# Performance work log

Hardware: AMD Instinct MI355X
Metric: run time of the kernel (lower is better)

The kernel has to match this reference:

```python
import jax, jax.numpy as jnp
import numpy as np

TAU = 0.2
EPS_NORM = 1e-12  # torch F.normalize eps


def _l2_normalize(x):
    n = jnp.linalg.norm(x, axis=-1, keepdims=True)
    return x / jnp.maximum(n, EPS_NORM)


def setup_inputs() -> dict:
    key = jax.random.key(0)
    k1, k2 = jax.random.split(key)
    seg_emb = jax.random.normal(k1, (131072, 512), dtype=jnp.float32)
    prototypes = jax.random.normal(k2, (64, 512), dtype=jnp.float32) * 0.02
    return {"seg_emb": seg_emb, "prototypes": prototypes}


def reference(seg_emb, prototypes):
    # normalize -> cosine-sim matmul -> temperature scale -> softmax -> weighted proto sum
    p = _l2_normalize(prototypes)          # [K, D]
    z = _l2_normalize(seg_emb)             # [N, D]
    logits = jnp.einsum('nd,kd->nk', z, p) / max(TAU, 1e-06)  # [N, K]
    w = jax.nn.softmax(logits, axis=-1)    # [N, K]
    pattern = jnp.einsum('nk,kd->nd', w, prototypes)           # [N, D]
    return pattern, w, logits
```

## Files before the change

### kernel.cpp

```cpp
#include <hip/hip_runtime.h>
#include <hip/hip_bf16.h>

typedef __attribute__((ext_vector_type(8))) short short8;
typedef __attribute__((ext_vector_type(4))) float f32x4;

#define NPROTO 64
#define DIM    512
#define TAU_INV 5.0f

__device__ __forceinline__ unsigned short f2bf(float f) {
    union { float f; unsigned int u; } v; v.f = f;
    unsigned int r = v.u + 0x7FFFu + ((v.u >> 16) & 1u);
    return (unsigned short)(r >> 16);
}

__global__ void pb_prep(const float* __restrict__ protos,
                        unsigned short* __restrict__ pnorm,
                        unsigned short* __restrict__ protosT) {
    const int k    = blockIdx.x;
    const int lane = threadIdx.x;
    const float* row = protos + k * DIM;
    float x[8];
    float ss = 0.0f;
#pragma unroll
    for (int j = 0; j < 8; ++j) {
        x[j] = row[lane * 8 + j];
        ss += x[j] * x[j];
    }
#pragma unroll
    for (int m = 1; m < 64; m <<= 1) ss += __shfl_xor(ss, m, 64);
    const float s = 1.0f / fmaxf(sqrtf(ss), 1e-12f);
    short8 pn;
#pragma unroll
    for (int j = 0; j < 8; ++j) pn[j] = (short)f2bf(x[j] * s);
    *reinterpret_cast<short8*>(pnorm + k * DIM + lane * 8) = pn;
#pragma unroll
    for (int j = 0; j < 8; ++j)
        protosT[(lane * 8 + j) * NPROTO + k] = f2bf(x[j]);
}

__global__ __launch_bounds__(256, 4) void pb_main(
    const float* __restrict__ seg,
    const unsigned short* __restrict__ pnorm,
    const unsigned short* __restrict__ protosT,
    float* __restrict__ out_pat,
    float* __restrict__ out_w,
    float* __restrict__ out_log) {

    __shared__ unsigned short wbuf_all[4 * 2 * 16 * 64];

    const int wid  = (int)(threadIdx.x >> 6);
    const int lane = (int)(threadIdx.x & 63);
    const int g    = lane >> 4;
    const int r16  = lane & 15;
    const long n0  = ((long)blockIdx.x * 4 + wid) * 32;

    f32x4 acc0[4] = {}, acc1[4] = {};
    float ss0 = 0.0f, ss1 = 0.0f;
    const float* ap0 = seg + (n0 + r16) * DIM + g * 8;
    const float* ap1 = ap0 + 16 * DIM;

    f32x4 a00 = *reinterpret_cast<const f32x4*>(ap0);
    f32x4 a01 = *reinterpret_cast<const f32x4*>(ap0 + 4);
    f32x4 a10 = *reinterpret_cast<const f32x4*>(ap1);
    f32x4 a11 = *reinterpret_cast<const f32x4*>(ap1 + 4);

#pragma unroll
    for (int kt = 0; kt < 16; ++kt) {
        f32x4 n00, n01, n10, n11;
        if (kt < 15) {
            n00 = *reinterpret_cast<const f32x4*>(ap0 + (kt + 1) * 32);
            n01 = *reinterpret_cast<const f32x4*>(ap0 + (kt + 1) * 32 + 4);
            n10 = *reinterpret_cast<const f32x4*>(ap1 + (kt + 1) * 32);
            n11 = *reinterpret_cast<const f32x4*>(ap1 + (kt + 1) * 32 + 4);
        }
        short8 af0, af1;
#pragma unroll
        for (int j = 0; j < 4; ++j) {
            ss0 += a00[j] * a00[j] + a01[j] * a01[j];
            ss1 += a10[j] * a10[j] + a11[j] * a11[j];
            af0[j] = (short)f2bf(a00[j]); af0[j + 4] = (short)f2bf(a01[j]);
            af1[j] = (short)f2bf(a10[j]); af1[j + 4] = (short)f2bf(a11[j]);
        }
        const unsigned short* bbase = pnorm + r16 * DIM + g * 8 + kt * 32;
#pragma unroll
        for (int c = 0; c < 4; ++c) {
            const short8 bf = *reinterpret_cast<const short8*>(bbase + c * 16 * DIM);
            acc0[c] = __builtin_amdgcn_mfma_f32_16x16x32_bf16(af0, bf, acc0[c], 0, 0, 0);
            acc1[c] = __builtin_amdgcn_mfma_f32_16x16x32_bf16(af1, bf, acc1[c], 0, 0, 0);
        }
        if (kt < 15) { a00 = n00; a01 = n01; a10 = n10; a11 = n11; }
    }

    ss0 += __shfl_xor(ss0, 16, 64); ss0 += __shfl_xor(ss0, 32, 64);
    ss1 += __shfl_xor(ss1, 16, 64); ss1 += __shfl_xor(ss1, 32, 64);
    const float sco0 = TAU_INV / fmaxf(sqrtf(ss0), 1e-12f);
    const float sco1 = TAU_INV / fmaxf(sqrtf(ss1), 1e-12f);
    float sc0[4], sc1[4];
#pragma unroll
    for (int q = 0; q < 4; ++q) {
        sc0[q] = __shfl(sco0, g * 4 + q, 64);
        sc1[q] = __shfl(sco1, g * 4 + q, 64);
    }

    float lg0[4][4], lg1[4][4];
#pragma unroll
    for (int c = 0; c < 4; ++c)
#pragma unroll
        for (int q = 0; q < 4; ++q) {
            lg0[c][q] = acc0[c][q] * sc0[q];
            lg1[c][q] = acc1[c][q] * sc1[q];
            out_log[(n0 + g * 4 + q) * NPROTO + c * 16 + r16]      = lg0[c][q];
            out_log[(n0 + 16 + g * 4 + q) * NPROTO + c * 16 + r16] = lg1[c][q];
        }

    float w0[4][4], w1[4][4];
#pragma unroll
    for (int q = 0; q < 4; ++q) {
        float mx0 = fmaxf(fmaxf(lg0[0][q], lg0[1][q]), fmaxf(lg0[2][q], lg0[3][q]));
        float mx1 = fmaxf(fmaxf(lg1[0][q], lg1[1][q]), fmaxf(lg1[2][q], lg1[3][q]));
#pragma unroll
        for (int msk = 1; msk < 16; msk <<= 1) {
            mx0 = fmaxf(mx0, __shfl_xor(mx0, msk, 64));
            mx1 = fmaxf(mx1, __shfl_xor(mx1, msk, 64));
        }
        float e0[4], e1[4], sum0 = 0.0f, sum1 = 0.0f;
#pragma unroll
        for (int c = 0; c < 4; ++c) {
            e0[c] = __expf(lg0[c][q] - mx0); sum0 += e0[c];
            e1[c] = __expf(lg1[c][q] - mx1); sum1 += e1[c];
        }
#pragma unroll
        for (int msk = 1; msk < 16; msk <<= 1) {
            sum0 += __shfl_xor(sum0, msk, 64);
            sum1 += __shfl_xor(sum1, msk, 64);
        }
        const float i0 = 1.0f / sum0, i1 = 1.0f / sum1;
#pragma unroll
        for (int c = 0; c < 4; ++c) { w0[c][q] = e0[c] * i0; w1[c][q] = e1[c] * i1; }
    }

    unsigned short* wb0 = wbuf_all + (wid * 2 + 0) * (16 * 64);
    unsigned short* wb1 = wbuf_all + (wid * 2 + 1) * (16 * 64);
#pragma unroll
    for (int c = 0; c < 4; ++c)
#pragma unroll
        for (int q = 0; q < 4; ++q) {
            out_w[(n0 + g * 4 + q) * NPROTO + c * 16 + r16]      = w0[c][q];
            out_w[(n0 + 16 + g * 4 + q) * NPROTO + c * 16 + r16] = w1[c][q];
            const int row  = g * 4 + q;
            const int col  = c * 16 + r16;
            const int byte = (row * 128 + col * 2) ^ ((row & 7) << 4);
            *reinterpret_cast<unsigned short*>(reinterpret_cast<char*>(wb0) + byte) = f2bf(w0[c][q]);
            *reinterpret_cast<unsigned short*>(reinterpret_cast<char*>(wb1) + byte) = f2bf(w1[c][q]);
        }

    __syncthreads();

    short8 wa[2][2];
    {
        const int row = r16;
        const int b0 = (row * 128 + g * 16)      ^ ((row & 7) << 4);
        const int b1 = (row * 128 + g * 16 + 64) ^ ((row & 7) << 4);
        wa[0][0] = *reinterpret_cast<const short8*>(reinterpret_cast<char*>(wb0) + b0);
        wa[0][1] = *reinterpret_cast<const short8*>(reinterpret_cast<char*>(wb0) + b1);
        wa[1][0] = *reinterpret_cast<const short8*>(reinterpret_cast<char*>(wb1) + b0);
        wa[1][1] = *reinterpret_cast<const short8*>(reinterpret_cast<char*>(wb1) + b1);
    }

#pragma unroll 2
    for (int cp = 0; cp < 32; ++cp) {
        const unsigned short* bp = protosT + (cp * 16 + r16) * NPROTO + g * 8;
        const short8 b0 = *reinterpret_cast<const short8*>(bp);
        const short8 b1 = *reinterpret_cast<const short8*>(bp + 32);
        f32x4 p0 = {}, p1 = {};
        p0 = __builtin_amdgcn_mfma_f32_16x16x32_bf16(wa[0][0], b0, p0, 0, 0, 0);
        p0 = __builtin_amdgcn_mfma_f32_16x16x32_bf16(wa[0][1], b1, p0, 0, 0, 0);
        p1 = __builtin_amdgcn_mfma_f32_16x16x32_bf16(wa[1][0], b0, p1, 0, 0, 0);
        p1 = __builtin_amdgcn_mfma_f32_16x16x32_bf16(wa[1][1], b1, p1, 0, 0, 0);
#pragma unroll
        for (int q = 0; q < 4; ++q) {
            out_pat[(n0 + g * 4 + q) * DIM + cp * 16 + r16]      = p0[q];
            out_pat[(n0 + 16 + g * 4 + q) * DIM + cp * 16 + r16] = p1[q];
        }
    }
}

extern "C" void kernel_launch(void* const* d_in, const int* in_sizes, int n_in,
                              void* d_out, int out_size, void* d_ws, size_t ws_size,
                              hipStream_t stream) {
    const float* seg    = (const float*)d_in[0];
    const float* protos = (const float*)d_in[1];
    const int N = in_sizes[0] / DIM;

    float* out     = (float*)d_out;
    float* out_pat = out;
    float* out_w   = out_pat + (size_t)N * DIM;
    float* out_log = out_w + (size_t)N * NPROTO;

    unsigned short* pnorm   = (unsigned short*)d_ws;
    unsigned short* protosT = pnorm + NPROTO * DIM;

    pb_prep<<<NPROTO, 64, 0, stream>>>(protos, pnorm, protosT);
    pb_main<<<N / 128, 256, 0, stream>>>(seg, pnorm, protosT, out_pat, out_w, out_log);
}
```

Before: 167.6 us.

## Use nontemporal loads/stores, smaller blocks, XCD-aware block remap, prefetch proto tiles

The main kernel now uses nontemporal loads for the embedding stream and nontemporal stores for all three outputs, to avoid polluting caches with single-use data. Blocks shrink from 4 to 2 waves, and block indices are remapped so that consecutive row chunks land on the same XCD. The redundant __syncthreads is removed, since each wave only reads its own LDS region. The transposed-prototype fragments are double-buffered in registers during the second matmul. The kernel is memory-bound, so most of the effect depends on how the cache hints and the block remap interact with HBM traffic. The remap silently assumes the grid size is a multiple of 8.

```diff
diff --git a/kernel.cpp b/kernel.cpp
--- a/kernel.cpp
+++ b/kernel.cpp
@@ -39,7 +39,7 @@
         protosT[(lane * 8 + j) * NPROTO + k] = f2bf(x[j]);
 }
 
-__global__ __launch_bounds__(256, 4) void pb_main(
+__global__ __launch_bounds__(128, 4) void pb_main(
     const float* __restrict__ seg,
     const unsigned short* __restrict__ pnorm,
     const unsigned short* __restrict__ protosT,
@@ -47,32 +47,36 @@
     float* __restrict__ out_w,
     float* __restrict__ out_log) {
 
-    __shared__ unsigned short wbuf_all[4 * 2 * 16 * 64];
+    __shared__ unsigned short wbuf_all[2 * 2 * 16 * 64];
 
     const int wid  = (int)(threadIdx.x >> 6);
     const int lane = (int)(threadIdx.x & 63);
     const int g    = lane >> 4;
     const int r16  = lane & 15;
-    const long n0  = ((long)blockIdx.x * 4 + wid) * 32;
+
+    const int nwg  = (int)gridDim.x;
+    const int cpx  = nwg >> 3;
+    const int blk  = ((int)blockIdx.x & 7) * cpx + ((int)blockIdx.x >> 3);
+    const long n0  = ((long)blk * 2 + wid) * 32;
 
     f32x4 acc0[4] = {}, acc1[4] = {};
     float ss0 = 0.0f, ss1 = 0.0f;
     const float* ap0 = seg + (n0 + r16) * DIM + g * 8;
     const float* ap1 = ap0 + 16 * DIM;
 
-    f32x4 a00 = *reinterpret_cast<const f32x4*>(ap0);
-    f32x4 a01 = *reinterpret_cast<const f32x4*>(ap0 + 4);
-    f32x4 a10 = *reinterpret_cast<const f32x4*>(ap1);
-    f32x4 a11 = *reinterpret_cast<const f32x4*>(ap1 + 4);
+    f32x4 a00 = __builtin_nontemporal_load(reinterpret_cast<const f32x4*>(ap0));
+    f32x4 a01 = __builtin_nontemporal_load(reinterpret_cast<const f32x4*>(ap0 + 4));
+    f32x4 a10 = __builtin_nontemporal_load(reinterpret_cast<const f32x4*>(ap1));
+    f32x4 a11 = __builtin_nontemporal_load(reinterpret_cast<const f32x4*>(ap1 + 4));
 
 #pragma unroll
     for (int kt = 0; kt < 16; ++kt) {
         f32x4 n00, n01, n10, n11;
         if (kt < 15) {
-            n00 = *reinterpret_cast<const f32x4*>(ap0 + (kt + 1) * 32);
-            n01 = *reinterpret_cast<const f32x4*>(ap0 + (kt + 1) * 32 + 4);
-            n10 = *reinterpret_cast<const f32x4*>(ap1 + (kt + 1) * 32);
-            n11 = *reinterpret_cast<const f32x4*>(ap1 + (kt + 1) * 32 + 4);
+            n00 = __builtin_nontemporal_load(reinterpret_cast<const f32x4*>(ap0 + (kt + 1) * 32));
+            n01 = __builtin_nontemporal_load(reinterpret_cast<const f32x4*>(ap0 + (kt + 1) * 32 + 4));
+            n10 = __builtin_nontemporal_load(reinterpret_cast<const f32x4*>(ap1 + (kt + 1) * 32));
+            n11 = __builtin_nontemporal_load(reinterpret_cast<const f32x4*>(ap1 + (kt + 1) * 32 + 4));
         }
         short8 af0, af1;
 #pragma unroll
@@ -110,8 +114,10 @@
         for (int q = 0; q < 4; ++q) {
             lg0[c][q] = acc0[c][q] * sc0[q];
             lg1[c][q] = acc1[c][q] * sc1[q];
-            out_log[(n0 + g * 4 + q) * NPROTO + c * 16 + r16]      = lg0[c][q];
-            out_log[(n0 + 16 + g * 4 + q) * NPROTO + c * 16 + r16] = lg1[c][q];
+            __builtin_nontemporal_store(lg0[c][q],
+                &out_log[(n0 + g * 4 + q) * NPROTO + c * 16 + r16]);
+            __builtin_nontemporal_store(lg1[c][q],
+                &out_log[(n0 + 16 + g * 4 + q) * NPROTO + c * 16 + r16]);
         }
 
     float w0[4][4], w1[4][4];
@@ -140,14 +146,16 @@
         for (int c = 0; c < 4; ++c) { w0[c][q] = e0[c] * i0; w1[c][q] = e1[c] * i1; }
     }
 
-    unsigned short* wb0 = wbuf_all + (wid * 2 + 0) * (16 * 64);
-    unsigned short* wb1 = wbuf_all + (wid * 2 + 1) * (16 * 64);
+    unsigned short* wb0 = wbuf_all + (wid * 2 + 0) * 1024;
+    unsigned short* wb1 = wbuf_all + (wid * 2 + 1) * 1024;
 #pragma unroll
     for (int c = 0; c < 4; ++c)
 #pragma unroll
         for (int q = 0; q < 4; ++q) {
-            out_w[(n0 + g * 4 + q) * NPROTO + c * 16 + r16]      = w0[c][q];
-            out_w[(n0 + 16 + g * 4 + q) * NPROTO + c * 16 + r16] = w1[c][q];
+            __builtin_nontemporal_store(w0[c][q],
+                &out_w[(n0 + g * 4 + q) * NPROTO + c * 16 + r16]);
+            __builtin_nontemporal_store(w1[c][q],
+                &out_w[(n0 + 16 + g * 4 + q) * NPROTO + c * 16 + r16]);
             const int row  = g * 4 + q;
             const int col  = c * 16 + r16;
             const int byte = (row * 128 + col * 2) ^ ((row & 7) << 4);
@@ -155,33 +163,38 @@
             *reinterpret_cast<unsigned short*>(reinterpret_cast<char*>(wb1) + byte) = f2bf(w1[c][q]);
         }
 
-    __syncthreads();
-
     short8 wa[2][2];
     {
-        const int row = r16;
-        const int b0 = (row * 128 + g * 16)      ^ ((row & 7) << 4);
-        const int b1 = (row * 128 + g * 16 + 64) ^ ((row & 7) << 4);
+        const int b0 = (r16 * 128 + g * 16)      ^ ((r16 & 7) << 4);
+        const int b1 = (r16 * 128 + g * 16 + 64) ^ ((r16 & 7) << 4);
         wa[0][0] = *reinterpret_cast<const short8*>(reinterpret_cast<char*>(wb0) + b0);
         wa[0][1] = *reinterpret_cast<const short8*>(reinterpret_cast<char*>(wb0) + b1);
         wa[1][0] = *reinterpret_cast<const short8*>(reinterpret_cast<char*>(wb1) + b0);
         wa[1][1] = *reinterpret_cast<const short8*>(reinterpret_cast<char*>(wb1) + b1);
     }
 
-#pragma unroll 2
+    short8 pbuf[2][2];
+    const unsigned short* btile = protosT + r16 * NPROTO + g * 8;
+    pbuf[0][0] = *reinterpret_cast<const short8*>(btile);
+    pbuf[0][1] = *reinterpret_cast<const short8*>(btile + 32);
+#pragma unroll
     for (int cp = 0; cp < 32; ++cp) {
-        const unsigned short* bp = protosT + (cp * 16 + r16) * NPROTO + g * 8;
-        const short8 b0 = *reinterpret_cast<const short8*>(bp);
-        const short8 b1 = *reinterpret_cast<const short8*>(bp + 32);
+        if (cp < 31) {
+            const unsigned short* bn = btile + (cp + 1) * 16 * NPROTO;
+            pbuf[(cp + 1) & 1][0] = *reinterpret_cast<const short8*>(bn);
+            pbuf[(cp + 1) & 1][1] = *reinterpret_cast<const short8*>(bn + 32);
+        }
         f32x4 p0 = {}, p1 = {};
-        p0 = __builtin_amdgcn_mfma_f32_16x16x32_bf16(wa[0][0], b0, p0, 0, 0, 0);
-        p0 = __builtin_amdgcn_mfma_f32_16x16x32_bf16(wa[0][1], b1, p0, 0, 0, 0);
-        p1 = __builtin_amdgcn_mfma_f32_16x16x32_bf16(wa[1][0], b0, p1, 0, 0, 0);
-        p1 = __builtin_amdgcn_mfma_f32_16x16x32_bf16(wa[1][1], b1, p1, 0, 0, 0);
+        p0 = __builtin_amdgcn_mfma_f32_16x16x32_bf16(wa[0][0], pbuf[cp & 1][0], p0, 0, 0, 0);
+        p0 = __builtin_amdgcn_mfma_f32_16x16x32_bf16(wa[0][1], pbuf[cp & 1][1], p0, 0, 0, 0);
+        p1 = __builtin_amdgcn_mfma_f32_16x16x32_bf16(wa[1][0], pbuf[cp & 1][0], p1, 0, 0, 0);
+        p1 = __builtin_amdgcn_mfma_f32_16x16x32_bf16(wa[1][1], pbuf[cp & 1][1], p1, 0, 0, 0);
 #pragma unroll
         for (int q = 0; q < 4; ++q) {
-            out_pat[(n0 + g * 4 + q) * DIM + cp * 16 + r16]      = p0[q];
-            out_pat[(n0 + 16 + g * 4 + q) * DIM + cp * 16 + r16] = p1[q];
+            __builtin_nontemporal_store(p0[q],
+                &out_pat[(n0 + g * 4 + q) * DIM + cp * 16 + r16]);
+            __builtin_nontemporal_store(p1[q],
+                &out_pat[(n0 + 16 + g * 4 + q) * DIM + cp * 16 + r16]);
         }
     }
 }
@@ -202,5 +215,5 @@
     unsigned short* protosT = pnorm + NPROTO * DIM;
 
     pb_prep<<<NPROTO, 64, 0, stream>>>(protos, pnorm, protosT);
-    pb_main<<<N / 128, 256, 0, stream>>>(seg, pnorm, protosT, out_pat, out_w, out_log);
-}
+    pb_main<<<N / 64, 128, 0, stream>>>(seg, pnorm, protosT, out_pat, out_w, out_log);
+}
```

New measurement: 186.5 us. 11.3% more time.
